# Optimization experiments

Measured on AMD Instinct MI355X. Metric: run time of the kernel, lower is better.

The kernel has to match this reference:

```python
import jax, jax.numpy as jnp
import numpy as np

B, L, D, Y = 8, 2500, 512, 8921

def setup_inputs() -> dict:
    key = jax.random.key(0)
    k1, k2, k3, k4 = jax.random.split(key, 4)
    x = jax.random.normal(k1, (B, L, D), dtype=jnp.float32)
    # xavier-ish init scale for the label-attention and output matrices
    scale = (2.0 / (Y + D)) ** 0.5
    U_w = jax.random.normal(k2, (Y, D), dtype=jnp.float32) * scale
    final_w = jax.random.normal(k3, (Y, D), dtype=jnp.float32) * scale
    final_b = jax.random.normal(k4, (Y,), dtype=jnp.float32) * 0.01
    return {"x": x, "U_w": U_w, "final_w": final_w, "final_b": final_b}

def reference(x, U_w, final_w, final_b):
    # scores[b, y, l] = U_w[y, :] . x[b, l, :]
    scores = jnp.einsum('yd,bld->byl', U_w, x)            # (B, Y, L)
    alpha = jax.nn.softmax(scores, axis=2)                 # softmax over seq dim
    m = jnp.einsum('byl,bld->byd', alpha, x)               # (B, Y, D)
    y = jnp.einsum('yd,byd->by', final_w, m) + final_b     # (B, Y)
    return y
```

## Files before the change

### kernel.cpp

```cpp
#include <hip/hip_runtime.h>
#include <hip/hip_bf16.h>

#define NB 8
#define NL 2500
#define ND 512
#define NY 8921

#define BM 256
#define BN 256
#define BK 32
#define NKS 16
#define LPAD 2560
#define NLT 10
#define NYB 70
#define YPAD 8960

#define SPLIT 5
#define LSPL_MAIN 2

#define TILE 16384
#define GT_BYTES ((size_t)NYB * NKS * TILE)
#define XT_BYTES ((size_t)NB * NLT * NKS * TILE)
#define P_ELEMS  ((size_t)SPLIT * NB * YPAD)
#define P_BYTES  (P_ELEMS * 4)

typedef short s8v __attribute__((ext_vector_type(8)));
typedef float f4v __attribute__((ext_vector_type(4)));

__device__ __forceinline__ unsigned short f2bf(float f) {
  unsigned int u = __float_as_uint(f);
  return (unsigned short)((u + 0x7FFFu + ((u >> 16) & 1u)) >> 16);
}
__device__ __forceinline__ unsigned int pk2(float a, float b) {
  return (unsigned int)f2bf(a) | ((unsigned int)f2bf(b) << 16);
}
__device__ __forceinline__ void async_copy16(const char* g, char* l) {
  __builtin_amdgcn_global_load_lds(
      (const __attribute__((address_space(1))) void*)g,
      (__attribute__((address_space(3))) void*)l, 16, 0, 0);
}

__device__ __forceinline__ int tile_off(int r, int gn) {
  int rp = r >> 1;
  return rp * 128 + ((((r & 1) << 6) | (gn << 4)) ^ ((rp & 7) << 4));
}

__global__ void cvt_g_kernel(const float* __restrict__ U, const float* __restrict__ W,
                             char* __restrict__ Gt) {
  int c = blockIdx.x * 256 + threadIdx.x;
  int g10 = c & 1023;
  int tile = c >> 10;
  int ks = tile & 15, yblk = tile >> 4;
  int r = g10 >> 2, gn = g10 & 3;
  int rg = yblk * 256 + r;
  int y = rg >> 1;
  uint4 o;
  if (y < NY) {
    const float* src = (rg & 1) ? W : U;
    const float4* p = (const float4*)(src + (size_t)y * ND + ks * BK + gn * 8);
    float4 f0 = p[0], f1 = p[1];
    o.x = pk2(f0.x, f0.y); o.y = pk2(f0.z, f0.w);
    o.z = pk2(f1.x, f1.y); o.w = pk2(f1.z, f1.w);
  } else {
    o = make_uint4(0u, 0u, 0u, 0u);
  }
  *(uint4*)(Gt + (size_t)tile * TILE + tile_off(r, gn)) = o;
}

__global__ void cvt_x_kernel(const float* __restrict__ x, char* __restrict__ Xt) {
  int c = blockIdx.x * 256 + threadIdx.x;
  int g10 = c & 1023;
  int tile = c >> 10;
  int ks = tile & 15, rest = tile >> 4;
  int t = rest % NLT, b = rest / NLT;
  int r = g10 >> 2, gn = g10 & 3;
  int l = t * 256 + r;
  uint4 o;
  if (l < NL) {
    const float4* p = (const float4*)(x + ((size_t)b * NL + l) * ND + ks * BK + gn * 8);
    float4 f0 = p[0], f1 = p[1];
    o.x = pk2(f0.x, f0.y); o.y = pk2(f0.z, f0.w);
    o.z = pk2(f1.x, f1.y); o.w = pk2(f1.z, f1.w);
  } else {
    o = make_uint4(0u, 0u, 0u, 0u);
  }
  *(uint4*)(Xt + (size_t)tile * TILE + tile_off(r, gn)) = o;
}

template<int LSPL, int NSPL, bool PARTIAL>
__global__ __launch_bounds__(512, 2) void fused_kernel(
    const char* __restrict__ Gt, const char* __restrict__ Xt,
    const float* __restrict__ bias, float* __restrict__ out,
    float* __restrict__ PD, float* __restrict__ PN)
{
  __shared__ uint4 ring[8192];
  char* ringC = (char*)ring;

  constexpr int NS = LSPL * NKS;

  const int tid  = threadIdx.x;
  const int lane = tid & 63;
  const int w    = tid >> 6;
  const int wr   = w >> 2;
  const int wc   = w & 3;
  const int cl   = lane & 15, g = lane >> 4;

  const int id    = blockIdx.x;
  const int bb    = id & 7;
  const int n     = id >> 3;
  const int yblk  = n / NSPL;
  const int split = n - yblk * NSPL;
  const int tbase = split * LSPL;

  const char* GA = Gt + (size_t)yblk * NKS * TILE;
  const char* XB = Xt + ((size_t)bb * NLT + tbase) * NKS * TILE;

  f4v acc[8][4];
  float runD[8][2], runN[8][2];
  #pragma unroll
  for (int mi = 0; mi < 8; ++mi)
    #pragma unroll
    for (int p = 0; p < 2; ++p) { runD[mi][p] = 0.f; runN[mi][p] = 0.f; }

  int aoff[8], boff[4];
  #pragma unroll
  for (int j = 0; j < 8; ++j) aoff[j] = tile_off(wr * 128 + j * 16 + cl, g);
  #pragma unroll
  for (int ni = 0; ni < 4; ++ni) boff[ni] = tile_off(wc * 64 + ni * 16 + cl, g);

  const int t16 = tid << 4;
  auto stageA = [&](int s) {
    const char* ga = GA + (size_t)(s & 15) * TILE;
    char* la = ringC + (s & 3) * TILE + (w << 10);
    async_copy16(ga + t16, la);
    async_copy16(ga + 8192 + t16, la + 8192);
  };
  auto stageB = [&](int s) {
    const char* gb = XB + (size_t)s * TILE;
    char* lb = ringC + 65536 + (s & 3) * TILE + (w << 10);
    async_copy16(gb + t16, lb);
    async_copy16(gb + 8192 + t16, lb + 8192);
  };

  stageA(0); stageB(0);
  stageA(1); stageB(1);
  stageA(2); stageB(2);
  asm volatile("s_waitcnt vmcnt(8)" ::: "memory");
  __builtin_amdgcn_s_barrier();
  asm volatile("" ::: "memory");

  for (int u = 0; u < NS; ++u) {
    const int ks = u & (NKS - 1);
    const char* A = ringC + (u & 3) * TILE;
    const char* B = ringC + 65536 + (u & 3) * TILE;
    const bool hn = (u + 3) < NS;

    if (ks == 0) {
      #pragma unroll
      for (int mi = 0; mi < 8; ++mi)
        #pragma unroll
        for (int ni = 0; ni < 4; ++ni)
          #pragma unroll
          for (int q = 0; q < 4; ++q) acc[mi][ni][q] = 0.f;
    }

    s8v bv[4], af[4];
    #pragma unroll
    for (int ni = 0; ni < 4; ++ni) bv[ni] = *(const s8v*)(B + boff[ni]);
    #pragma unroll
    for (int j = 0; j < 4; ++j)    af[j] = *(const s8v*)(A + aoff[j]);
    if (hn) stageA(u + 3);
    __builtin_amdgcn_s_barrier();
    asm volatile("s_waitcnt lgkmcnt(0)" ::: "memory");
    __builtin_amdgcn_sched_barrier(0);
    __builtin_amdgcn_s_setprio(1);
    #pragma unroll
    for (int j = 0; j < 4; ++j)
      #pragma unroll
      for (int ni = 0; ni < 4; ++ni)
        acc[j][ni] = __builtin_amdgcn_mfma_f32_16x16x32_bf16(af[j], bv[ni], acc[j][ni], 0, 0, 0);
    __builtin_amdgcn_s_setprio(0);
    __builtin_amdgcn_s_barrier();
    asm volatile("" ::: "memory");

    #pragma unroll
    for (int j = 0; j < 4; ++j) af[j] = *(const s8v*)(A + aoff[4 + j]);
    if (hn) stageB(u + 3);
    __builtin_amdgcn_s_barrier();
    asm volatile("s_waitcnt lgkmcnt(0)" ::: "memory");
    __builtin_amdgcn_sched_barrier(0);
    __builtin_amdgcn_s_setprio(1);
    #pragma unroll
    for (int j = 0; j < 4; ++j)
      #pragma unroll
      for (int ni = 0; ni < 4; ++ni)
        acc[4 + j][ni] = __builtin_amdgcn_mfma_f32_16x16x32_bf16(af[j], bv[ni], acc[4 + j][ni], 0, 0, 0);
    __builtin_amdgcn_s_setprio(0);

    if (ks == NKS - 1) {
      const int lbase = (tbase + (u >> 4)) * BN + wc * 64 + cl;
      #pragma unroll
      for (int mi = 0; mi < 8; ++mi) {
        #pragma unroll
        for (int p = 0; p < 2; ++p) {
          float se = 0.f, ste = 0.f;
          #pragma unroll
          for (int ni = 0; ni < 4; ++ni) {
            bool valid = (lbase + ni * 16) < NL;
            float sv = valid ? acc[mi][ni][2 * p] : -1e30f;
            float e = __expf(sv);
            se += e;
            ste += e * acc[mi][ni][2 * p + 1];
          }
          runD[mi][p] += se;
          runN[mi][p] += ste;
        }
      }
    }

    if (u <= NS - 4) {
      asm volatile("s_waitcnt vmcnt(8)" ::: "memory");
    } else if (u == NS - 3) {
      asm volatile("s_waitcnt vmcnt(4)" ::: "memory");
    } else if (u == NS - 2) {
      asm volatile("s_waitcnt vmcnt(0)" ::: "memory");
    }
    __builtin_amdgcn_s_barrier();
    asm volatile("" ::: "memory");
  }

  #pragma unroll
  for (int mi = 0; mi < 8; ++mi)
    #pragma unroll
    for (int p = 0; p < 2; ++p) {
      float d = runD[mi][p], nn = runN[mi][p];
      #pragma unroll
      for (int off = 1; off < 16; off <<= 1) {
        d += __shfl_xor(d, off);
        nn += __shfl_xor(nn, off);
      }
      runD[mi][p] = d; runN[mi][p] = nn;
    }

  __syncthreads();
  float* sm = (float*)ring;
  if (cl == 0) {
    #pragma unroll
    for (int mi = 0; mi < 8; ++mi)
      #pragma unroll
      for (int p = 0; p < 2; ++p) {
        int lab = wr * 64 + mi * 8 + 2 * g + p;
        float* s2 = sm + (lab * 4 + wc) * 2;
        s2[0] = runD[mi][p]; s2[1] = runN[mi][p];
      }
  }
  __syncthreads();
  if (tid < 128) {
    float D = 0.f, N = 0.f;
    #pragma unroll
    for (int q = 0; q < 4; ++q) {
      const float* s2 = sm + (tid * 4 + q) * 2;
      D += s2[0]; N += s2[1];
    }
    int y = yblk * 128 + tid;
    if constexpr (PARTIAL) {
      size_t o = ((size_t)split * NB + bb) * YPAD + y;
      PD[o] = D; PN[o] = N;
    } else {
      if (y < NY) out[(size_t)bb * NY + y] = N / D + bias[y];
    }
  }
}

__global__ void merge_kernel(const float* __restrict__ PD, const float* __restrict__ PN,
                             const float* __restrict__ bias, float* __restrict__ out) {
  int idx = blockIdx.x * 256 + threadIdx.x;
  int b = idx / YPAD, y = idx - b * YPAD;
  if (y >= NY) return;
  float D = 0.f, N = 0.f;
  #pragma unroll
  for (int s = 0; s < SPLIT; ++s) {
    size_t o = ((size_t)s * NB + b) * YPAD + y;
    D += PD[o];
    N += PN[o];
  }
  out[(size_t)b * NY + y] = N / D + bias[y];
}

extern "C" void kernel_launch(void* const* d_in, const int* in_sizes, int n_in,
                              void* d_out, int out_size, void* d_ws, size_t ws_size,
                              hipStream_t stream) {
  const float* xf   = (const float*)d_in[0];
  const float* Uf   = (const float*)d_in[1];
  const float* Wf   = (const float*)d_in[2];
  const float* bias = (const float*)d_in[3];
  float* out = (float*)d_out;

  char* Gt = (char*)d_ws;
  char* Xt = Gt + GT_BYTES;
  float* PD = (float*)(Xt + XT_BYTES);
  float* PN = PD + P_ELEMS;

  cvt_g_kernel<<<4480, 256, 0, stream>>>(Uf, Wf, Gt);
  cvt_x_kernel<<<5120, 256, 0, stream>>>(xf, Xt);

  const size_t need_main = GT_BYTES + XT_BYTES + 2 * P_BYTES;
  if (ws_size >= need_main) {
    fused_kernel<LSPL_MAIN, SPLIT, true><<<NYB * NB * SPLIT, 512, 0, stream>>>(
        Gt, Xt, bias, out, PD, PN);
    merge_kernel<<<NB * YPAD / 256, 256, 0, stream>>>(PD, PN, bias, out);
  } else {
    fused_kernel<NLT, 1, false><<<NYB * NB, 512, 0, stream>>>(
        Gt, Xt, bias, out, PD, PN);
  }
}
```

Before: 398.8 us.

## Software-pipeline LDS fragment loads and cut per-step barriers in the GEMM loop

Restructures the main K loop so that the LDS fragments for the next step are loaded into alternating register sets while the current step's MFMAs run. The loop is unrolled by two through a macro to make this double buffering possible. Both global-to-LDS stages are now issued together at the start of each step, and the three block barriers per step drop to one, with vmcnt waits retuned to match. This hides LDS latency and cuts sync overhead, at the cost of extra registers that may reduce occupancy and of relying on NS being even.

```diff
diff --git a/kernel.cpp b/kernel.cpp
--- a/kernel.cpp
+++ b/kernel.cpp
@@ -145,89 +145,97 @@
   stageA(0); stageB(0);
   stageA(1); stageB(1);
   stageA(2); stageB(2);
-  asm volatile("s_waitcnt vmcnt(8)" ::: "memory");
+  asm volatile("s_waitcnt vmcnt(4)" ::: "memory");
   __builtin_amdgcn_s_barrier();
   asm volatile("" ::: "memory");
 
-  for (int u = 0; u < NS; ++u) {
-    const int ks = u & (NKS - 1);
-    const char* A = ringC + (u & 3) * TILE;
-    const char* B = ringC + 65536 + (u & 3) * TILE;
-    const bool hn = (u + 3) < NS;
-
-    if (ks == 0) {
-      #pragma unroll
-      for (int mi = 0; mi < 8; ++mi)
-        #pragma unroll
-        for (int ni = 0; ni < 4; ++ni)
-          #pragma unroll
-          for (int q = 0; q < 4; ++q) acc[mi][ni][q] = 0.f;
-    }
-
-    s8v bv[4], af[4];
-    #pragma unroll
-    for (int ni = 0; ni < 4; ++ni) bv[ni] = *(const s8v*)(B + boff[ni]);
-    #pragma unroll
-    for (int j = 0; j < 4; ++j)    af[j] = *(const s8v*)(A + aoff[j]);
-    if (hn) stageA(u + 3);
-    __builtin_amdgcn_s_barrier();
-    asm volatile("s_waitcnt lgkmcnt(0)" ::: "memory");
-    __builtin_amdgcn_sched_barrier(0);
-    __builtin_amdgcn_s_setprio(1);
-    #pragma unroll
-    for (int j = 0; j < 4; ++j)
-      #pragma unroll
-      for (int ni = 0; ni < 4; ++ni)
-        acc[j][ni] = __builtin_amdgcn_mfma_f32_16x16x32_bf16(af[j], bv[ni], acc[j][ni], 0, 0, 0);
-    __builtin_amdgcn_s_setprio(0);
-    __builtin_amdgcn_s_barrier();
-    asm volatile("" ::: "memory");
-
-    #pragma unroll
-    for (int j = 0; j < 4; ++j) af[j] = *(const s8v*)(A + aoff[4 + j]);
-    if (hn) stageB(u + 3);
-    __builtin_amdgcn_s_barrier();
-    asm volatile("s_waitcnt lgkmcnt(0)" ::: "memory");
-    __builtin_amdgcn_sched_barrier(0);
-    __builtin_amdgcn_s_setprio(1);
-    #pragma unroll
-    for (int j = 0; j < 4; ++j)
-      #pragma unroll
-      for (int ni = 0; ni < 4; ++ni)
-        acc[4 + j][ni] = __builtin_amdgcn_mfma_f32_16x16x32_bf16(af[j], bv[ni], acc[4 + j][ni], 0, 0, 0);
-    __builtin_amdgcn_s_setprio(0);
-
-    if (ks == NKS - 1) {
-      const int lbase = (tbase + (u >> 4)) * BN + wc * 64 + cl;
-      #pragma unroll
-      for (int mi = 0; mi < 8; ++mi) {
-        #pragma unroll
-        for (int p = 0; p < 2; ++p) {
-          float se = 0.f, ste = 0.f;
-          #pragma unroll
-          for (int ni = 0; ni < 4; ++ni) {
-            bool valid = (lbase + ni * 16) < NL;
-            float sv = valid ? acc[mi][ni][2 * p] : -1e30f;
-            float e = __expf(sv);
-            se += e;
-            ste += e * acc[mi][ni][2 * p + 1];
-          }
-          runD[mi][p] += se;
-          runN[mi][p] += ste;
-        }
-      }
-    }
-
-    if (u <= NS - 4) {
-      asm volatile("s_waitcnt vmcnt(8)" ::: "memory");
-    } else if (u == NS - 3) {
-      asm volatile("s_waitcnt vmcnt(4)" ::: "memory");
-    } else if (u == NS - 2) {
-      asm volatile("s_waitcnt vmcnt(0)" ::: "memory");
-    }
-    __builtin_amdgcn_s_barrier();
-    asm volatile("" ::: "memory");
-  }
+  s8v bvA[4], afA[4], bvB[4], afB[4], a47[4];
+  {
+    const char* A0 = ringC;
+    const char* B0 = ringC + 65536;
+    #pragma unroll
+    for (int ni = 0; ni < 4; ++ni) bvA[ni] = *(const s8v*)(B0 + boff[ni]);
+    #pragma unroll
+    for (int j = 0; j < 4; ++j)    afA[j] = *(const s8v*)(A0 + aoff[j]);
+  }
+
+#define K_STEP(U, CBV, CAF, NBV, NAF)                                          \
+  do {                                                                         \
+    const int u_  = (U);                                                       \
+    const int ks_ = u_ & (NKS - 1);                                            \
+    const char* A_ = ringC + (u_ & 3) * TILE;                                  \
+    if (ks_ == 0) {                                                            \
+      _Pragma("unroll")                                                        \
+      for (int mi = 0; mi < 8; ++mi)                                           \
+        _Pragma("unroll")                                                      \
+        for (int ni = 0; ni < 4; ++ni)                                         \
+          _Pragma("unroll")                                                    \
+          for (int q = 0; q < 4; ++q) acc[mi][ni][q] = 0.f;                    \
+    }                                                                          \
+    if (u_ + 3 < NS) { stageA(u_ + 3); stageB(u_ + 3); }                       \
+    _Pragma("unroll")                                                          \
+    for (int j = 0; j < 4; ++j) a47[j] = *(const s8v*)(A_ + aoff[4 + j]);      \
+    __builtin_amdgcn_sched_barrier(0);                                         \
+    __builtin_amdgcn_s_setprio(1);                                             \
+    _Pragma("unroll")                                                          \
+    for (int j = 0; j < 4; ++j)                                                \
+      _Pragma("unroll")                                                        \
+      for (int ni = 0; ni < 4; ++ni)                                           \
+        acc[j][ni] = __builtin_amdgcn_mfma_f32_16x16x32_bf16(                  \
+            CAF[j], CBV[ni], acc[j][ni], 0, 0, 0);                             \
+    __builtin_amdgcn_s_setprio(0);                                             \
+    __builtin_amdgcn_sched_barrier(0);                                         \
+    if (u_ + 1 < NS) {                                                         \
+      const char* An_ = ringC + ((u_ + 1) & 3) * TILE;                         \
+      const char* Bn_ = ringC + 65536 + ((u_ + 1) & 3) * TILE;                 \
+      _Pragma("unroll")                                                        \
+      for (int ni = 0; ni < 4; ++ni) NBV[ni] = *(const s8v*)(Bn_ + boff[ni]);  \
+      _Pragma("unroll")                                                        \
+      for (int j = 0; j < 4; ++j)    NAF[j] = *(const s8v*)(An_ + aoff[j]);    \
+    }                                                                          \
+    __builtin_amdgcn_sched_barrier(0);                                         \
+    __builtin_amdgcn_s_setprio(1);                                             \
+    _Pragma("unroll")                                                          \
+    for (int j = 0; j < 4; ++j)                                                \
+      _Pragma("unroll")                                                        \
+      for (int ni = 0; ni < 4; ++ni)                                           \
+        acc[4 + j][ni] = __builtin_amdgcn_mfma_f32_16x16x32_bf16(              \
+            a47[j], CBV[ni], acc[4 + j][ni], 0, 0, 0);                         \
+    __builtin_amdgcn_s_setprio(0);                                             \
+    if (ks_ == NKS - 1) {                                                      \
+      const int lbase = (tbase + (u_ >> 4)) * BN + wc * 64 + cl;               \
+      _Pragma("unroll")                                                        \
+      for (int mi = 0; mi < 8; ++mi) {                                         \
+        _Pragma("unroll")                                                      \
+        for (int p = 0; p < 2; ++p) {                                          \
+          float se = 0.f, ste = 0.f;                                           \
+          _Pragma("unroll")                                                    \
+          for (int ni = 0; ni < 4; ++ni) {                                     \
+            bool valid = (lbase + ni * 16) < NL;                               \
+            float sv = valid ? acc[mi][ni][2 * p] : -1e30f;                    \
+            float e = __expf(sv);                                              \
+            se += e;                                                           \
+            ste += e * acc[mi][ni][2 * p + 1];                                 \
+          }                                                                    \
+          runD[mi][p] += se;                                                   \
+          runN[mi][p] += ste;                                                  \
+        }                                                                      \
+      }                                                                        \
+    }                                                                          \
+    if (u_ <= NS - 4) {                                                        \
+      asm volatile("s_waitcnt vmcnt(4)" ::: "memory");                         \
+    } else if (u_ == NS - 3) {                                                 \
+      asm volatile("s_waitcnt vmcnt(0)" ::: "memory");                         \
+    }                                                                          \
+    __builtin_amdgcn_s_barrier();                                              \
+    asm volatile("" ::: "memory");                                             \
+  } while (0)
+
+  for (int uu = 0; uu < NS; uu += 2) {
+    K_STEP(uu,     bvA, afA, bvB, afB);
+    K_STEP(uu + 1, bvB, afB, bvA, afA);
+  }
+#undef K_STEP
 
   #pragma unroll
   for (int mi = 0; mi < 8; ++mi)
```

After: 375.6 us. 1.06x faster.

## Restructure GEMM main loop into ping-pong double-buffered k-pairs with register prefetch

Applied to the files above, without the earlier changes.

The main loop now processes two K-slices per iteration, using two 32KB ring halves for A and B as a double buffer instead of a four-deep single-slice ring. LDS fragment loads for the next MFMA group are issued before the current MFMA group, so ds_read latency overlaps with matrix math. Waits use partial lgkmcnt/vmcnt counts. The softmax accumulation moves to the start of the next L tile. This cuts prefetch depth from three stages to one pair ahead and adds more barriers per iteration, which could expose global-load latency.

```diff
diff --git a/kernel.cpp b/kernel.cpp
--- a/kernel.cpp
+++ b/kernel.cpp
@@ -96,7 +96,7 @@
   __shared__ uint4 ring[8192];
   char* ringC = (char*)ring;
 
-  constexpr int NS = LSPL * NKS;
+  constexpr int NKT = LSPL * 8;
 
   const int tid  = threadIdx.x;
   const int lane = tid & 63;
@@ -129,33 +129,66 @@
   for (int ni = 0; ni < 4; ++ni) boff[ni] = tile_off(wc * 64 + ni * 16 + cl, g);
 
   const int t16 = tid << 4;
-  auto stageA = [&](int s) {
-    const char* ga = GA + (size_t)(s & 15) * TILE;
-    char* la = ringC + (s & 3) * TILE + (w << 10);
+  auto stgA = [&](int kt1, int par) {
+    const char* ga = GA + (size_t)((((kt1 & 7) << 1) | par)) * TILE;
+    char* la = ringC + (kt1 & 1) * 32768 + par * 16384 + (w << 10);
     async_copy16(ga + t16, la);
     async_copy16(ga + 8192 + t16, la + 8192);
   };
-  auto stageB = [&](int s) {
-    const char* gb = XB + (size_t)s * TILE;
-    char* lb = ringC + 65536 + (s & 3) * TILE + (w << 10);
+  auto stgB = [&](int kt1, int par) {
+    const char* gb = XB + (size_t)((kt1 >> 3) * 16 + ((kt1 & 7) << 1) + par) * TILE;
+    char* lb = ringC + 65536 + (kt1 & 1) * 32768 + par * 16384 + (w << 10);
     async_copy16(gb + t16, lb);
     async_copy16(gb + 8192 + t16, lb + 8192);
   };
 
-  stageA(0); stageB(0);
-  stageA(1); stageB(1);
-  stageA(2); stageB(2);
-  asm volatile("s_waitcnt vmcnt(8)" ::: "memory");
+  auto softmax_acc = [&](int tt) {
+    const int lbase = (tbase + tt) * BN + wc * 64 + cl;
+    #pragma unroll
+    for (int mi = 0; mi < 8; ++mi) {
+      #pragma unroll
+      for (int p = 0; p < 2; ++p) {
+        float se = 0.f, ste = 0.f;
+        #pragma unroll
+        for (int ni = 0; ni < 4; ++ni) {
+          bool valid = (lbase + ni * 16) < NL;
+          float sv = valid ? acc[mi][ni][2 * p] : -1e30f;
+          float e = __expf(sv);
+          se += e;
+          ste += e * acc[mi][ni][2 * p + 1];
+        }
+        runD[mi][p] += se;
+        runN[mi][p] += ste;
+      }
+    }
+  };
+
+#define SBAR __builtin_amdgcn_sched_barrier(0)
+#define LGKM(N) asm volatile("s_waitcnt lgkmcnt(" #N ")" ::: "memory")
+#define VMC(N)  asm volatile("s_waitcnt vmcnt(" #N ")" ::: "memory")
+
+  stgA(0, 0); stgB(0, 0); stgA(0, 1); stgB(0, 1);
+  VMC(4);
   __builtin_amdgcn_s_barrier();
   asm volatile("" ::: "memory");
 
-  for (int u = 0; u < NS; ++u) {
-    const int ks = u & (NKS - 1);
-    const char* A = ringC + (u & 3) * TILE;
-    const char* B = ringC + 65536 + (u & 3) * TILE;
-    const bool hn = (u + 3) < NS;
-
-    if (ks == 0) {
+  s8v bvE[4], bvO[4], afX[4], afY[4];
+  #pragma unroll
+  for (int ni = 0; ni < 4; ++ni) bvE[ni] = *(const s8v*)(ringC + 65536 + boff[ni]);
+  #pragma unroll
+  for (int j = 0; j < 4; ++j)    afX[j] = *(const s8v*)(ringC + aoff[j]);
+
+  for (int kt = 0; kt < NKT; ++kt) {
+    const int buf = kt & 1;
+    const char* Ae = ringC + buf * 32768;
+    const char* Ao = Ae + 16384;
+    const char* Bo = ringC + 65536 + buf * 32768 + 16384;
+    const char* Aen = ringC + (buf ^ 1) * 32768;
+    const char* Ben = ringC + 65536 + (buf ^ 1) * 32768;
+    const bool hn = (kt + 1) < NKT;
+
+    if ((kt & 7) == 0) {
+      if (kt > 0) softmax_acc((kt >> 3) - 1);
       #pragma unroll
       for (int mi = 0; mi < 8; ++mi)
         #pragma unroll
@@ -164,70 +197,91 @@
           for (int q = 0; q < 4; ++q) acc[mi][ni][q] = 0.f;
     }
 
-    s8v bv[4], af[4];
-    #pragma unroll
-    for (int ni = 0; ni < 4; ++ni) bv[ni] = *(const s8v*)(B + boff[ni]);
-    #pragma unroll
-    for (int j = 0; j < 4; ++j)    af[j] = *(const s8v*)(A + aoff[j]);
-    if (hn) stageA(u + 3);
-    __builtin_amdgcn_s_barrier();
-    asm volatile("s_waitcnt lgkmcnt(0)" ::: "memory");
-    __builtin_amdgcn_sched_barrier(0);
+    if (hn) stgA(kt + 1, 0);
+    #pragma unroll
+    for (int j = 0; j < 4; ++j) afY[j] = *(const s8v*)(Ae + aoff[4 + j]);
+    SBAR;
+    __builtin_amdgcn_s_barrier();
+    LGKM(4); SBAR;
     __builtin_amdgcn_s_setprio(1);
     #pragma unroll
     for (int j = 0; j < 4; ++j)
       #pragma unroll
       for (int ni = 0; ni < 4; ++ni)
-        acc[j][ni] = __builtin_amdgcn_mfma_f32_16x16x32_bf16(af[j], bv[ni], acc[j][ni], 0, 0, 0);
+        acc[j][ni] = __builtin_amdgcn_mfma_f32_16x16x32_bf16(afX[j], bvE[ni], acc[j][ni], 0, 0, 0);
     __builtin_amdgcn_s_setprio(0);
+    if (hn) { VMC(2); } else { VMC(0); }
+    SBAR;
     __builtin_amdgcn_s_barrier();
     asm volatile("" ::: "memory");
 
-    #pragma unroll
-    for (int j = 0; j < 4; ++j) af[j] = *(const s8v*)(A + aoff[4 + j]);
-    if (hn) stageB(u + 3);
-    __builtin_amdgcn_s_barrier();
-    asm volatile("s_waitcnt lgkmcnt(0)" ::: "memory");
-    __builtin_amdgcn_sched_barrier(0);
+    if (hn) stgB(kt + 1, 0);
+    #pragma unroll
+    for (int ni = 0; ni < 4; ++ni) bvO[ni] = *(const s8v*)(Bo + boff[ni]);
+    #pragma unroll
+    for (int j = 0; j < 4; ++j)    afX[j] = *(const s8v*)(Ao + aoff[j]);
+    SBAR;
+    __builtin_amdgcn_s_barrier();
+    LGKM(8); SBAR;
     __builtin_amdgcn_s_setprio(1);
     #pragma unroll
     for (int j = 0; j < 4; ++j)
       #pragma unroll
       for (int ni = 0; ni < 4; ++ni)
-        acc[4 + j][ni] = __builtin_amdgcn_mfma_f32_16x16x32_bf16(af[j], bv[ni], acc[4 + j][ni], 0, 0, 0);
+        acc[4 + j][ni] = __builtin_amdgcn_mfma_f32_16x16x32_bf16(afY[j], bvE[ni], acc[4 + j][ni], 0, 0, 0);
     __builtin_amdgcn_s_setprio(0);
-
-    if (ks == NKS - 1) {
-      const int lbase = (tbase + (u >> 4)) * BN + wc * 64 + cl;
-      #pragma unroll
-      for (int mi = 0; mi < 8; ++mi) {
-        #pragma unroll
-        for (int p = 0; p < 2; ++p) {
-          float se = 0.f, ste = 0.f;
-          #pragma unroll
-          for (int ni = 0; ni < 4; ++ni) {
-            bool valid = (lbase + ni * 16) < NL;
-            float sv = valid ? acc[mi][ni][2 * p] : -1e30f;
-            float e = __expf(sv);
-            se += e;
-            ste += e * acc[mi][ni][2 * p + 1];
-          }
-          runD[mi][p] += se;
-          runN[mi][p] += ste;
-        }
-      }
-    }
-
-    if (u <= NS - 4) {
-      asm volatile("s_waitcnt vmcnt(8)" ::: "memory");
-    } else if (u == NS - 3) {
-      asm volatile("s_waitcnt vmcnt(4)" ::: "memory");
-    } else if (u == NS - 2) {
-      asm volatile("s_waitcnt vmcnt(0)" ::: "memory");
-    }
+    SBAR;
     __builtin_amdgcn_s_barrier();
     asm volatile("" ::: "memory");
-  }
+
+    if (hn) stgA(kt + 1, 1);
+    #pragma unroll
+    for (int j = 0; j < 4; ++j) afY[j] = *(const s8v*)(Ao + aoff[4 + j]);
+    SBAR;
+    __builtin_amdgcn_s_barrier();
+    LGKM(4); SBAR;
+    __builtin_amdgcn_s_setprio(1);
+    #pragma unroll
+    for (int j = 0; j < 4; ++j)
+      #pragma unroll
+      for (int ni = 0; ni < 4; ++ni)
+        acc[j][ni] = __builtin_amdgcn_mfma_f32_16x16x32_bf16(afX[j], bvO[ni], acc[j][ni], 0, 0, 0);
+    __builtin_amdgcn_s_setprio(0);
+    if (hn) VMC(2);
+    SBAR;
+    __builtin_amdgcn_s_barrier();
+    asm volatile("" ::: "memory");
+
+    if (hn) {
+      stgB(kt + 1, 1);
+      #pragma unroll
+      for (int ni = 0; ni < 4; ++ni) bvE[ni] = *(const s8v*)(Ben + boff[ni]);
+      #pragma unroll
+      for (int j = 0; j < 4; ++j)    afX[j] = *(const s8v*)(Aen + aoff[j]);
+      SBAR;
+      __builtin_amdgcn_s_barrier();
+      LGKM(8); SBAR;
+    } else {
+      SBAR;
+      __builtin_amdgcn_s_barrier();
+      LGKM(0); SBAR;
+    }
+    __builtin_amdgcn_s_setprio(1);
+    #pragma unroll
+    for (int j = 0; j < 4; ++j)
+      #pragma unroll
+      for (int ni = 0; ni < 4; ++ni)
+        acc[4 + j][ni] = __builtin_amdgcn_mfma_f32_16x16x32_bf16(afY[j], bvO[ni], acc[4 + j][ni], 0, 0, 0);
+    __builtin_amdgcn_s_setprio(0);
+    SBAR;
+    __builtin_amdgcn_s_barrier();
+    asm volatile("" ::: "memory");
+  }
+  softmax_acc(LSPL - 1);
+
+#undef SBAR
+#undef LGKM
+#undef VMC
 
   #pragma unroll
   for (int mi = 0; mi < 8; ++mi)
```

New measurement: 361.6 us (median of 2 runs). -9.3%, faster.
